# Kernel tuning notes

Measured on AMD Instinct MI355X. Metric: run time of the kernel, lower is better.

## Reference

```python
import jax, jax.numpy as jnp
import numpy as np

B, T, D, H = 64, 2048, 512, 512


def setup_inputs() -> dict:
    key = jax.random.key(0)
    ks = jax.random.split(key, 10)
    seq_tensor = jax.random.normal(ks[0], (B, T, D), dtype=jnp.float32)
    # pack_padded_sequence semantics: lengths sorted descending, max length == T
    lens = jax.random.randint(ks[1], (B,), 1, T + 1)
    lens = jnp.sort(lens)[::-1].at[0].set(T).astype(jnp.int32)
    u = lambda k, s: jax.random.uniform(k, s, jnp.float32, -0.08, 0.08)
    return {
        "seq_tensor": seq_tensor,
        "seq_lengths": lens,
        "W_i2h": u(ks[2], (2 * H, D)), "b_i2h": u(ks[3], (2 * H,)),
        "W_h2h": u(ks[4], (2 * H, H)), "b_h2h": u(ks[5], (2 * H,)),
        "W_i2o": u(ks[6], (H, D)), "b_i2o": u(ks[7], (H,)),
        "W_h2o": u(ks[8], (H, H)), "b_h2o": u(ks[9], (H,)),
    }


def reference(seq_tensor, seq_lengths, W_i2h, b_i2h, W_h2h, b_h2h,
              W_i2o, b_i2o, W_h2o, b_h2o):
    # Precompute all input projections in one big GEMM each (hoisted out of the recurrence)
    x_zr = jnp.einsum('btd,kd->btk', seq_tensor, W_i2h) + b_i2h   # [B,T,2H]
    x_o = jnp.einsum('btd,hd->bth', seq_tensor, W_i2o) + b_i2o    # [B,T,H]
    steps = jnp.arange(seq_tensor.shape[1])
    hidden = W_h2o.shape[0]

    def step(prev_h, inp):
        xzr_t, xo_t, t = inp
        preact = xzr_t + prev_h @ W_h2h.T + b_h2h                 # [B,2H]
        z, r = jnp.split(preact, 2, axis=-1)
        s = xo_t + (prev_h * jax.nn.sigmoid(r)) @ W_h2o.T + b_h2o
        zs = jax.nn.sigmoid(z)
        h = (1.0 - zs) * prev_h + zs * jnp.tanh(s)
        mask = (t < seq_lengths)[:, None]                         # active (ragged) rows
        new_h = jnp.where(mask, h, prev_h)                        # freeze finished rows
        out = jnp.where(mask, h, jnp.zeros_like(h))               # zero-padded output
        return new_h, out

    h0 = jnp.zeros((seq_tensor.shape[0], hidden), seq_tensor.dtype)
    final_h, outs = jax.lax.scan(
        step, h0,
        (x_zr.transpose(1, 0, 2), x_o.transpose(1, 0, 2), steps))
    outputs = outs.transpose(1, 0, 2)                              # [B,T,H]
    return outputs, final_h[None]                                  # final_state = (1,B,H)
```

## Files before the change

kernel.cpp:

```cpp
#include <hip/hip_runtime.h>
#include <stdint.h>


typedef _Float16 h8_t __attribute__((ext_vector_type(8)));
typedef float    f4_t __attribute__((ext_vector_type(4)));
typedef unsigned long long u64;

#define NB   64
#define NT   2048
#define ND   512
#define NH   512
#define NROW (NB * NT)
#define NCOL 1536
#define NGRP 4
#define NSL  16
#define WPAD 520

static const size_t OFF_P   = 0;
static const size_t OFF_WC  = (size_t)NROW * NCOL * 2;
static const size_t OFF_WHH = OFF_WC  + (size_t)1536 * 512 * 2;
static const size_t OFF_WHO = OFF_WHH + (size_t)1024 * 512 * 2;
static const size_t OFF_CB  = OFF_WHO + (size_t)512 * 512 * 2;
static const size_t OFF_HC  = OFF_CB  + 1536 * 4;
static const size_t OFF_GC  = OFF_HC  + (size_t)NB * 512 * 2;
static const size_t OFF_FL  = OFF_GC  + (size_t)NB * 512 * 2;
static const size_t FL_SZ   = (size_t)2 * NGRP * (NT + 1) * 4;

__global__ void pack_kernel(const float* __restrict__ Wi2h, const float* __restrict__ bi2h,
                            const float* __restrict__ Wh2h, const float* __restrict__ bh2h,
                            const float* __restrict__ Wi2o, const float* __restrict__ bi2o,
                            const float* __restrict__ Wh2o, const float* __restrict__ bh2o,
                            _Float16* __restrict__ Wc, _Float16* __restrict__ Whh,
                            _Float16* __restrict__ Who, float* __restrict__ cbias)
{
    int id = blockIdx.x * 256 + threadIdx.x;
    if (id < 786432) {
        int n = id >> 9;
        float v = (n < 1024) ? Wi2h[id] : Wi2o[id - 524288];
        Wc[id] = (_Float16)v;
    } else if (id < 786432 + 524288) {
        int lid = id - 786432;
        Whh[lid] = (_Float16)Wh2h[lid];
    } else if (id < 786432 + 524288 + 262144) {
        int lid = id - 1310720;
        Who[lid] = (_Float16)Wh2o[lid];
    } else if (id < 1572864 + 1536) {
        int n = id - 1572864;
        cbias[n] = (n < 1024) ? (bi2h[n] + bh2h[n]) : (bi2o[n - 1024] + bh2o[n - 1024]);
    }
}

__global__ void gemm_proj(const float* __restrict__ X, const _Float16* __restrict__ Wc,
                          const float* __restrict__ cbias, const int* __restrict__ lens,
                          _Float16* __restrict__ P)
{
    int bid  = blockIdx.x;
    int xcd  = bid & 7;
    int slot = bid >> 3;
    int nt   = slot % 12;
    int tyl  = slot / 12;
    int ty   = xcd * 128 + tyl;

    int b  = ty >> 4;
    int t0 = (ty << 7) & 2047;
    if (t0 >= lens[b]) return;

    int rowbase = ty << 7;
    int nbase   = nt << 7;

    __shared__ _Float16 As[128][40];
    __shared__ _Float16 Bs[128][40];

    int tid  = threadIdx.x;
    int lane = tid & 63, w = tid >> 6;
    int wm = w >> 1, wn = w & 1;
    int fr = lane & 15, quad = lane >> 4;

    f4_t acc[4][4] = {};

    int sr = tid >> 2;
    int sc = (tid & 3) << 3;

    for (int kc = 0; kc < 16; ++kc) {
        int k0 = kc << 5;
#pragma unroll
        for (int p = 0; p < 2; ++p) {
            int r = sr + p * 64;
            const float* asrc = X + (size_t)(rowbase + r) * 512 + k0 + sc;
            f4_t a0 = *(const f4_t*)asrc;
            f4_t a1 = *(const f4_t*)(asrc + 4);
            h8_t hv;
            hv[0] = (_Float16)a0[0]; hv[1] = (_Float16)a0[1];
            hv[2] = (_Float16)a0[2]; hv[3] = (_Float16)a0[3];
            hv[4] = (_Float16)a1[0]; hv[5] = (_Float16)a1[1];
            hv[6] = (_Float16)a1[2]; hv[7] = (_Float16)a1[3];
            *(h8_t*)&As[r][sc] = hv;
            *(h8_t*)&Bs[r][sc] = *(const h8_t*)(Wc + (size_t)(nbase + r) * 512 + k0 + sc);
        }
        __syncthreads();

        h8_t af[4], bf[4];
#pragma unroll
        for (int i = 0; i < 4; ++i) {
            af[i] = *(const h8_t*)&As[wm * 64 + i * 16 + fr][quad * 8];
            bf[i] = *(const h8_t*)&Bs[wn * 64 + i * 16 + fr][quad * 8];
        }
#pragma unroll
        for (int mi = 0; mi < 4; ++mi)
#pragma unroll
            for (int ni = 0; ni < 4; ++ni)
                acc[mi][ni] = __builtin_amdgcn_mfma_f32_16x16x32_f16(
                    af[mi], bf[ni], acc[mi][ni], 0, 0, 0);
        __syncthreads();
    }

#pragma unroll
    for (int ni = 0; ni < 4; ++ni) {
        int gcol = nbase + wn * 64 + ni * 16 + fr;
        float bias = cbias[gcol];
#pragma unroll
        for (int mi = 0; mi < 4; ++mi) {
            int grow0 = rowbase + wm * 64 + mi * 16 + quad * 4;
#pragma unroll
            for (int rg = 0; rg < 4; ++rg)
                P[(size_t)(grow0 + rg) * NCOL + gcol] = (_Float16)(acc[mi][ni][rg] + bias);
        }
    }
}

__global__ __launch_bounds__(256)
void gru_rec(const _Float16* __restrict__ P,
             const _Float16* __restrict__ Whh,
             const _Float16* __restrict__ Who,
             const int* __restrict__ lens,
             float* __restrict__ out,
             _Float16* __restrict__ hcom,
             _Float16* __restrict__ gcom,
             unsigned int* __restrict__ flags)
{
    const int g    = blockIdx.x >> 4;
    const int s    = blockIdx.x & 15;
    const int tid  = threadIdx.x;
    const int lane = tid & 63;
    const int w    = tid >> 6;
    const int fr   = lane & 15;
    const int quad = lane >> 4;

    __shared__ _Float16 Wzr[64][WPAD];
    __shared__ _Float16 Wso[32][WPAD];
    __shared__ _Float16 hst[16][WPAD];
    __shared__ _Float16 gst[16][WPAD];
    __shared__ float    hloc[16][32];
    __shared__ _Float16 hout[16][32];
    __shared__ _Float16 gout[16][32];

    unsigned int* hflg = flags + g * (NT + 1);
    unsigned int* gflg = flags + (NGRP + g) * (NT + 1);

    for (int idx = tid; idx < 96 * 64; idx += 256) {
        int r = idx >> 6, ch = idx & 63;
        if (r < 64) {
            int grow = (r < 32) ? (s * 32 + r) : (512 + s * 32 + r - 32);
            *(uint4*)&Wzr[r][ch * 8] = ((const uint4*)(Whh + (size_t)grow * 512))[ch];
        } else {
            int grow = s * 32 + r - 64;
            *(uint4*)&Wso[r - 64][ch * 8] = ((const uint4*)(Who + (size_t)grow * 512))[ch];
        }
    }

    int    lrow[4];
    size_t pbase[4], obase[4];
    int    row_[4];
#pragma unroll
    for (int rg = 0; rg < 4; ++rg) {
        int row  = quad * 4 + rg;
        row_[rg] = row;
        int brow = g * 16 + row;
        lrow[rg]  = lens[brow];
        pbase[rg] = (size_t)brow * NT * NCOL;
        obase[rg] = (size_t)brow * NT * NH;
    }
    int steps = 0;
    for (int i = 0; i < 16; ++i) { int l = lens[g * 16 + i]; if (l > steps) steps = l; }

    float hreg[4] = {0.f, 0.f, 0.f, 0.f};
    float zreg[4] = {0.f, 0.f, 0.f, 0.f};

    const int lcol01 = w * 16 + fr;
    const int gcol01 = s * 32 + lcol01;
    const int rl23   = (w - 2) * 16 + fr;
    const int pcolr  = 512 + s * 32 + rl23;

    if (w < 2) {
#pragma unroll
        for (int rg = 0; rg < 4; ++rg) hloc[row_[rg]][lcol01] = 0.f;
    }
    if (tid < 128) {
        int r = tid >> 3, c = tid & 7;
        __hip_atomic_store((u64*)(hcom + (size_t)(g * 16 + r) * 512 + s * 32) + c,
                           0ull, __ATOMIC_RELAXED, __HIP_MEMORY_SCOPE_AGENT);
    }
    asm volatile("s_waitcnt vmcnt(0)" ::: "memory");
    __syncthreads();
    if (tid == 0)
        __hip_atomic_fetch_add(&hflg[0], 1u, __ATOMIC_RELEASE, __HIP_MEMORY_SCOPE_AGENT);

    for (int t = 0; t < steps; ++t) {
        if (tid == 0)
            while (__hip_atomic_load(&hflg[t], __ATOMIC_RELAXED,
                                     __HIP_MEMORY_SCOPE_AGENT) < (unsigned)NSL)
                __builtin_amdgcn_s_sleep(1);
        __syncthreads();

        _Float16 pzv[4], pov[4];
        const size_t tofs = (size_t)t * NCOL;
        if (w < 2) {
#pragma unroll
            for (int rg = 0; rg < 4; ++rg) {
                pzv[rg] = P[pbase[rg] + tofs + gcol01];
                pov[rg] = P[pbase[rg] + tofs + 1024 + gcol01];
            }
        } else {
#pragma unroll
            for (int rg = 0; rg < 4; ++rg)
                pzv[rg] = P[pbase[rg] + tofs + pcolr];
        }

#pragma unroll
        for (int i = 0; i < 8; ++i) {
            int idx = tid + i * 256;
            int r = idx >> 7, c4 = idx & 127;
            u64 v = __hip_atomic_load((u64*)(hcom + (size_t)(g * 16 + r) * 512) + c4,
                                      __ATOMIC_RELAXED, __HIP_MEMORY_SCOPE_AGENT);
            *(u64*)&hst[r][c4 * 4] = v;
        }
        __syncthreads();

        f4_t a0 = {0.f, 0.f, 0.f, 0.f}, a1 = {0.f, 0.f, 0.f, 0.f};
#pragma unroll
        for (int k = 0; k < 16; k += 2) {
            h8_t af0 = *(const h8_t*)&hst[fr][k * 32 + quad * 8];
            h8_t bf0 = *(const h8_t*)&Wzr[w * 16 + fr][k * 32 + quad * 8];
            a0 = __builtin_amdgcn_mfma_f32_16x16x32_f16(af0, bf0, a0, 0, 0, 0);
            h8_t af1 = *(const h8_t*)&hst[fr][(k + 1) * 32 + quad * 8];
            h8_t bf1 = *(const h8_t*)&Wzr[w * 16 + fr][(k + 1) * 32 + quad * 8];
            a1 = __builtin_amdgcn_mfma_f32_16x16x32_f16(af1, bf1, a1, 0, 0, 0);
        }

        if (w < 2) {
#pragma unroll
            for (int rg = 0; rg < 4; ++rg)
                zreg[rg] = a0[rg] + a1[rg] + (float)pzv[rg];
        } else {
#pragma unroll
            for (int rg = 0; rg < 4; ++rg) {
                float rv = a0[rg] + a1[rg] + (float)pzv[rg];
                float sg = 1.f / (1.f + __expf(-rv));
                gout[row_[rg]][rl23] = (_Float16)(hloc[row_[rg]][rl23] * sg);
            }
        }
        __syncthreads();

        if (tid < 128) {
            int r = tid >> 3, c = tid & 7;
            u64 v = *(const u64*)&gout[r][c * 4];
            __hip_atomic_store((u64*)(gcom + (size_t)(g * 16 + r) * 512 + s * 32) + c,
                               v, __ATOMIC_RELAXED, __HIP_MEMORY_SCOPE_AGENT);
        }
        asm volatile("s_waitcnt vmcnt(0)" ::: "memory");
        __syncthreads();
        if (tid == 0)
            __hip_atomic_fetch_add(&gflg[t], 1u, __ATOMIC_RELEASE, __HIP_MEMORY_SCOPE_AGENT);

        if (tid == 0)
            while (__hip_atomic_load(&gflg[t], __ATOMIC_RELAXED,
                                     __HIP_MEMORY_SCOPE_AGENT) < (unsigned)NSL)
                __builtin_amdgcn_s_sleep(1);
        __syncthreads();

#pragma unroll
        for (int i = 0; i < 8; ++i) {
            int idx = tid + i * 256;
            int r = idx >> 7, c4 = idx & 127;
            u64 v = __hip_atomic_load((u64*)(gcom + (size_t)(g * 16 + r) * 512) + c4,
                                      __ATOMIC_RELAXED, __HIP_MEMORY_SCOPE_AGENT);
            *(u64*)&gst[r][c4 * 4] = v;
        }
        __syncthreads();

        if (w < 2) {
            f4_t b0 = {0.f, 0.f, 0.f, 0.f}, b1 = {0.f, 0.f, 0.f, 0.f};
#pragma unroll
            for (int k = 0; k < 16; k += 2) {
                h8_t af0 = *(const h8_t*)&gst[fr][k * 32 + quad * 8];
                h8_t bf0 = *(const h8_t*)&Wso[w * 16 + fr][k * 32 + quad * 8];
                b0 = __builtin_amdgcn_mfma_f32_16x16x32_f16(af0, bf0, b0, 0, 0, 0);
                h8_t af1 = *(const h8_t*)&gst[fr][(k + 1) * 32 + quad * 8];
                h8_t bf1 = *(const h8_t*)&Wso[w * 16 + fr][(k + 1) * 32 + quad * 8];
                b1 = __builtin_amdgcn_mfma_f32_16x16x32_f16(af1, bf1, b1, 0, 0, 0);
            }
#pragma unroll
            for (int rg = 0; rg < 4; ++rg) {
                float sv = b0[rg] + b1[rg] + (float)pov[rg];
                float zs = 1.f / (1.f + __expf(-zreg[rg]));
                float th = 1.f - 2.f / (__expf(2.f * sv) + 1.f);
                float hn = (1.f - zs) * hreg[rg] + zs * th;
                bool act  = t < lrow[rg];
                float hc  = act ? hn : hreg[rg];
                out[obase[rg] + (size_t)t * NH + gcol01] = act ? hn : 0.f;
                hreg[rg] = hc;
                hloc[row_[rg]][lcol01] = hc;
                hout[row_[rg]][lcol01] = (_Float16)hc;
            }
        }
        __syncthreads();

        if (tid < 128) {
            int r = tid >> 3, c = tid & 7;
            u64 v = *(const u64*)&hout[r][c * 4];
            __hip_atomic_store((u64*)(hcom + (size_t)(g * 16 + r) * 512 + s * 32) + c,
                               v, __ATOMIC_RELAXED, __HIP_MEMORY_SCOPE_AGENT);
        }
        asm volatile("s_waitcnt vmcnt(0)" ::: "memory");
        __syncthreads();
        if (tid == 0)
            __hip_atomic_fetch_add(&hflg[t + 1], 1u, __ATOMIC_RELEASE, __HIP_MEMORY_SCOPE_AGENT);
    }

    if (w < 2) {
#pragma unroll
        for (int rg = 0; rg < 4; ++rg)
            out[(size_t)NB * NT * NH + (size_t)(g * 16 + row_[rg]) * NH + gcol01] = hreg[rg];
    }

    {
        long n4 = (long)(NT - steps) * 128;
        f4_t* dst = (f4_t*)(out + (size_t)(g * 16 + s) * NT * NH + (size_t)steps * NH);
        f4_t z = {0.f, 0.f, 0.f, 0.f};
        for (long i = tid; i < n4; i += 256) dst[i] = z;
    }
}

extern "C" void kernel_launch(void* const* d_in, const int* in_sizes, int n_in,
                              void* d_out, int out_size, void* d_ws, size_t ws_size,
                              hipStream_t stream)
{
    const float* X    = (const float*)d_in[0];
    const int*  lens  = (const int*)d_in[1];
    const float* Wi2h = (const float*)d_in[2];
    const float* bi2h = (const float*)d_in[3];
    const float* Wh2h = (const float*)d_in[4];
    const float* bh2h = (const float*)d_in[5];
    const float* Wi2o = (const float*)d_in[6];
    const float* bi2o = (const float*)d_in[7];
    const float* Wh2o = (const float*)d_in[8];
    const float* bh2o = (const float*)d_in[9];

    char* ws = (char*)d_ws;
    _Float16* P    = (_Float16*)(ws + OFF_P);
    _Float16* Wc   = (_Float16*)(ws + OFF_WC);
    _Float16* Whh  = (_Float16*)(ws + OFF_WHH);
    _Float16* Who  = (_Float16*)(ws + OFF_WHO);
    float*    cb   = (float*)(ws + OFF_CB);
    _Float16* hcom = (_Float16*)(ws + OFF_HC);
    _Float16* gcom = (_Float16*)(ws + OFF_GC);
    unsigned int* flags = (unsigned int*)(ws + OFF_FL);
    float* out = (float*)d_out;

    hipMemsetAsync(ws + OFF_FL, 0, FL_SZ, stream);

    pack_kernel<<<6150, 256, 0, stream>>>(Wi2h, bi2h, Wh2h, bh2h,
                                          Wi2o, bi2o, Wh2o, bh2o,
                                          Wc, Whh, Who, cb);
    gemm_proj<<<12288, 256, 0, stream>>>(X, Wc, cb, lens, P);
    gru_rec<<<NGRP * NSL, 256, 0, stream>>>(P, Whh, Who, lens, out, hcom, gcom, flags);
}
```

Baseline: 20.74 ms.

## Replace atomic counter barriers with per-slice flags and direct global stores

Swaps the per-step fetch_add counters for per-slice monotonic flag words, each padded into its own 64-byte slot. A single wavefront polls all 16 slice flags in parallel and checks them with __all. The h and g results are now stored straight to global memory with 16-bit atomic stores, which drops the LDS staging buffer and one __syncthreads per phase. The P prefetch is also moved ahead of the barrier wait. The cost is many more small 2-byte global stores, and the release ordering on the flags is now relaxed, relying only on the vmcnt wait.

```diff
diff --git a/kernel.cpp b/kernel.cpp
--- a/kernel.cpp
+++ b/kernel.cpp
@@ -24,7 +24,7 @@
 static const size_t OFF_HC  = OFF_CB  + 1536 * 4;
 static const size_t OFF_GC  = OFF_HC  + (size_t)NB * 512 * 2;
 static const size_t OFF_FL  = OFF_GC  + (size_t)NB * 512 * 2;
-static const size_t FL_SZ   = (size_t)2 * NGRP * (NT + 1) * 4;
+static const size_t FL_SZ   = (size_t)2 * NGRP * NSL * 16 * 4;
 
 __global__ void pack_kernel(const float* __restrict__ Wi2h, const float* __restrict__ bi2h,
                             const float* __restrict__ Wh2h, const float* __restrict__ bh2h,
@@ -151,11 +151,9 @@
     __shared__ _Float16 hst[16][WPAD];
     __shared__ _Float16 gst[16][WPAD];
     __shared__ float    hloc[16][32];
-    __shared__ _Float16 hout[16][32];
-    __shared__ _Float16 gout[16][32];
-
-    unsigned int* hflg = flags + g * (NT + 1);
-    unsigned int* gflg = flags + (NGRP + g) * (NT + 1);
+
+    unsigned int* hfl = flags + (size_t)g * 256;
+    unsigned int* gfl = flags + (size_t)(NGRP + g) * 256;
 
     for (int idx = tid; idx < 96 * 64; idx += 256) {
         int r = idx >> 6, ch = idx & 63;
@@ -203,17 +201,13 @@
     asm volatile("s_waitcnt vmcnt(0)" ::: "memory");
     __syncthreads();
     if (tid == 0)
-        __hip_atomic_fetch_add(&hflg[0], 1u, __ATOMIC_RELEASE, __HIP_MEMORY_SCOPE_AGENT);
+        __hip_atomic_store(&hfl[s * 16], 1u, __ATOMIC_RELAXED, __HIP_MEMORY_SCOPE_AGENT);
 
     for (int t = 0; t < steps; ++t) {
-        if (tid == 0)
-            while (__hip_atomic_load(&hflg[t], __ATOMIC_RELAXED,
-                                     __HIP_MEMORY_SCOPE_AGENT) < (unsigned)NSL)
-                __builtin_amdgcn_s_sleep(1);
-        __syncthreads();
+        const unsigned need = (unsigned)(t + 1);
+        const size_t tofs = (size_t)t * NCOL;
 
         _Float16 pzv[4], pov[4];
-        const size_t tofs = (size_t)t * NCOL;
         if (w < 2) {
 #pragma unroll
             for (int rg = 0; rg < 4; ++rg) {
@@ -225,6 +219,16 @@
             for (int rg = 0; rg < 4; ++rg)
                 pzv[rg] = P[pbase[rg] + tofs + pcolr];
         }
+
+        if (tid < 64) {
+            for (;;) {
+                unsigned v = __hip_atomic_load(&hfl[(lane & 15) * 16],
+                                               __ATOMIC_RELAXED, __HIP_MEMORY_SCOPE_AGENT);
+                if (__all(v >= need)) break;
+                __builtin_amdgcn_s_sleep(1);
+            }
+        }
+        __syncthreads();
 
 #pragma unroll
         for (int i = 0; i < 8; ++i) {
@@ -256,26 +260,25 @@
             for (int rg = 0; rg < 4; ++rg) {
                 float rv = a0[rg] + a1[rg] + (float)pzv[rg];
                 float sg = 1.f / (1.f + __expf(-rv));
-                gout[row_[rg]][rl23] = (_Float16)(hloc[row_[rg]][rl23] * sg);
-            }
-        }
-        __syncthreads();
-
-        if (tid < 128) {
-            int r = tid >> 3, c = tid & 7;
-            u64 v = *(const u64*)&gout[r][c * 4];
-            __hip_atomic_store((u64*)(gcom + (size_t)(g * 16 + r) * 512 + s * 32) + c,
-                               v, __ATOMIC_RELAXED, __HIP_MEMORY_SCOPE_AGENT);
+                _Float16 gv = (_Float16)(hloc[row_[rg]][rl23] * sg);
+                __hip_atomic_store((unsigned short*)(gcom +
+                        (size_t)(g * 16 + row_[rg]) * 512 + s * 32 + rl23),
+                    *(unsigned short*)&gv, __ATOMIC_RELAXED, __HIP_MEMORY_SCOPE_AGENT);
+            }
         }
         asm volatile("s_waitcnt vmcnt(0)" ::: "memory");
         __syncthreads();
         if (tid == 0)
-            __hip_atomic_fetch_add(&gflg[t], 1u, __ATOMIC_RELEASE, __HIP_MEMORY_SCOPE_AGENT);
-
-        if (tid == 0)
-            while (__hip_atomic_load(&gflg[t], __ATOMIC_RELAXED,
-                                     __HIP_MEMORY_SCOPE_AGENT) < (unsigned)NSL)
+            __hip_atomic_store(&gfl[s * 16], need, __ATOMIC_RELAXED, __HIP_MEMORY_SCOPE_AGENT);
+
+        if (tid < 64) {
+            for (;;) {
+                unsigned v = __hip_atomic_load(&gfl[(lane & 15) * 16],
+                                               __ATOMIC_RELAXED, __HIP_MEMORY_SCOPE_AGENT);
+                if (__all(v >= need)) break;
                 __builtin_amdgcn_s_sleep(1);
+            }
+        }
         __syncthreads();
 
 #pragma unroll
@@ -310,21 +313,16 @@
                 out[obase[rg] + (size_t)t * NH + gcol01] = act ? hn : 0.f;
                 hreg[rg] = hc;
                 hloc[row_[rg]][lcol01] = hc;
-                hout[row_[rg]][lcol01] = (_Float16)hc;
-            }
-        }
-        __syncthreads();
-
-        if (tid < 128) {
-            int r = tid >> 3, c = tid & 7;
-            u64 v = *(const u64*)&hout[r][c * 4];
-            __hip_atomic_store((u64*)(hcom + (size_t)(g * 16 + r) * 512 + s * 32) + c,
-                               v, __ATOMIC_RELAXED, __HIP_MEMORY_SCOPE_AGENT);
+                _Float16 hv = (_Float16)hc;
+                __hip_atomic_store((unsigned short*)(hcom +
+                        (size_t)(g * 16 + row_[rg]) * 512 + gcol01),
+                    *(unsigned short*)&hv, __ATOMIC_RELAXED, __HIP_MEMORY_SCOPE_AGENT);
+            }
         }
         asm volatile("s_waitcnt vmcnt(0)" ::: "memory");
         __syncthreads();
         if (tid == 0)
-            __hip_atomic_fetch_add(&hflg[t + 1], 1u, __ATOMIC_RELEASE, __HIP_MEMORY_SCOPE_AGENT);
+            __hip_atomic_store(&hfl[s * 16], need + 1, __ATOMIC_RELAXED, __HIP_MEMORY_SCOPE_AGENT);
     }
 
     if (w < 2) {
```

New measurement: 17.30 ms. 1.2x faster.
